# Kernel tuning notes

Measured on AMD Instinct MI355X. Metric: run time of the kernel, lower is better.

The kernel has to match this reference:

```python
import jax, jax.numpy as jnp
import numpy as np

B, H, S, D = 2, 12, 2048, 64

def setup_inputs() -> dict:
    key = jax.random.key(0)
    kq, kk, kv = jax.random.split(key, 3)
    Q = jax.random.normal(kq, (B, H, S, D), dtype=jnp.float32)
    K = jax.random.normal(kk, (B, H, S, D), dtype=jnp.float32)
    V = jax.random.normal(kv, (B, H, S, D), dtype=jnp.float32)
    return {"Q": Q, "K": K, "V": V}

def reference(Q, K, V):
    # NOTE: original code scales by sqrt(Q.shape[-2]) (the sequence length),
    # not the head dim — reproduced faithfully.
    scale = 1.0 / np.sqrt(Q.shape[-2]).astype(np.float32)
    scores = jnp.einsum('bhqd,bhkd->bhqk', Q, K) * scale  # [B,H,S,S]
    attn = jax.nn.softmax(scores, axis=-1)
    context = jnp.einsum('bhqk,bhkd->bhqd', attn, V)      # [B,H,S,D]
    # torch .squeeze(-1) only removes the last dim if it is size 1; D=64 so no-op
    return context
```

## Files before the change

kernel.cpp:

```cpp
#include <hip/hip_runtime.h>
#include <hip/hip_bf16.h>
#include <math.h>
#include <stdint.h>

#define BATCH 2
#define NH 12
#define SEQ 2048
#define HD 64
#define TQ 64
#define TK 64
#define NHEADS (BATCH*NH)
#define NIT (SEQ / TK)

typedef short bf16x8 __attribute__((ext_vector_type(8)));
typedef float f32x4 __attribute__((ext_vector_type(4)));
typedef float f32x16 __attribute__((ext_vector_type(16)));
typedef unsigned short us4_t __attribute__((ext_vector_type(4)));
typedef unsigned short us8_t __attribute__((ext_vector_type(8)));
typedef unsigned int u32x4 __attribute__((ext_vector_type(4)));

#if __has_builtin(__builtin_amdgcn_exp2f)
#define EXP2F(x) __builtin_amdgcn_exp2f(x)
#else
#define EXP2F(x) exp2f(x)
#endif

static __device__ __forceinline__ unsigned short f2bf(float f) {
    unsigned int u = __float_as_uint(f);
    u += 0x7fffu + ((u >> 16) & 1u);
    return (unsigned short)(u >> 16);
}

static __device__ __forceinline__ unsigned int pack2bf(float a, float b) {
    __hip_bfloat162 v = __float22bfloat162_rn(float2{a, b});
    return *(unsigned int*)&v;
}

static __device__ __forceinline__ void async_cp16(const void* g, void* l) {
    __builtin_amdgcn_global_load_lds(
        (const __attribute__((address_space(1))) void*)g,
        (__attribute__((address_space(3))) void*)(uintptr_t)l,
        16, 0, 0);
}

static __device__ __forceinline__ int tile_off(int r, int c) {
    int rp  = r >> 1;
    int pos = (((r & 1) << 3) | c) ^ (rp & 15);
    return rp * 128 + pos * 8;
}

__global__ __launch_bounds__(256)
void prep_kv(const float* __restrict__ K, const float* __restrict__ V,
             unsigned short* __restrict__ Kb, unsigned short* __restrict__ Vtb) {
    __shared__ unsigned short T[64][66];
    const int bh = blockIdx.x >> 5;
    const int s0 = (blockIdx.x & 31) * 64;
    const int tid = threadIdx.x;
    const size_t off = ((size_t)bh * SEQ + s0) * HD;

    #pragma unroll
    for (int u = 0; u < 4; ++u) {
        int idx = u * 1024 + tid * 4;
        float4 a = *(const float4*)&K[off + idx];
        us4_t r4 = { f2bf(a.x), f2bf(a.y), f2bf(a.z), f2bf(a.w) };
        *(us4_t*)&Kb[off + idx] = r4;
    }
    #pragma unroll
    for (int u = 0; u < 4; ++u) {
        int idx = u * 1024 + tid * 4;
        int r = idx >> 6, col = idx & 63;
        float4 a = *(const float4*)&V[off + idx];
        *(unsigned int*)&T[r][col]     = pack2bf(a.x, a.y);
        *(unsigned int*)&T[r][col + 2] = pack2bf(a.z, a.w);
    }
    __syncthreads();
    unsigned short* Vdst = Vtb + (size_t)bh * HD * SEQ;
    const int g = tid & 7, dd = tid >> 3;
    #pragma unroll
    for (int h = 0; h < 2; ++h) {
        int d = dd + 32 * h;
        us8_t r8;
        #pragma unroll
        for (int j = 0; j < 8; ++j) {
            int src = ((g >> 1) << 4) + ((j >> 2) << 3) + ((g & 1) << 2) + (j & 3);
            r8[j] = T[src][d];
        }
        *(us8_t*)&Vdst[(size_t)d * SEQ + s0 + g * 8] = r8;
    }
}

__global__ __launch_bounds__(256, 3)
void fa_main(const float* __restrict__ Q,
             const unsigned short* __restrict__ Kb,
             const unsigned short* __restrict__ Vtb,
             float* __restrict__ O, float qs) {
    const int x  = blockIdx.x & 7;
    const int t  = blockIdx.x >> 3;
    const int bh = x + 8 * (t % 3);
    const int qt = t / 3;
    const int q0 = qt * TQ;

    __shared__ __align__(16) unsigned char SH[49664];
    float* Lsum = (float*)(SH + 49152);
    float* Linv = (float*)(SH + 49408);
    float* ORed = (float*)SH;
    unsigned short* QS = (unsigned short*)(SH + 32768);

    const int tid  = threadIdx.x;
    const int w    = tid >> 6;
    const int mt   = w >> 1;
    const int nt   = w & 1;
    const int lane = tid & 63;
    const int l31  = lane & 31;
    const int hi   = lane >> 5;

    const float*          Qh = Q   + ((size_t)bh * SEQ + q0) * HD;
    const unsigned short* Kh = Kb  + (size_t)bh * SEQ * HD;
    const unsigned short* Vh = Vtb + (size_t)bh * HD * SEQ;

    int rS[2], cS[2];
    #pragma unroll
    for (int i = 0; i < 2; ++i) {
        int rp = w * 8 + 4 * i + (lane >> 4);
        int lc = (lane & 15) ^ (rp & 15);
        rS[i] = 2 * rp + (lc >> 3);
        cS[i] = lc & 7;
    }
    const int dst0 = (w * 8 + 0) * 128, dst1 = (w * 8 + 4) * 128;
    const size_t kG0 = (size_t)rS[0] * HD  + cS[0] * 8;
    const size_t kG1 = (size_t)rS[1] * HD  + cS[1] * 8;
    const size_t vG0 = (size_t)rS[0] * SEQ + cS[0] * 8;
    const size_t vG1 = (size_t)rS[1] * SEQ + cS[1] * 8;

    {
        unsigned short* K0 = (unsigned short*)(SH);
        unsigned short* V0 = (unsigned short*)(SH + 8192);
        async_cp16(Kh + kG0, &K0[dst0]);
        async_cp16(Kh + kG1, &K0[dst1]);
        async_cp16(Vh + vG0, &V0[dst0]);
        async_cp16(Vh + vG1, &V0[dst1]);
    }
    #pragma unroll
    for (int u = 0; u < 4; ++u) {
        int idx = u * 1024 + tid * 4;
        int r = idx >> 6, col = idx & 63;
        float4 a = *(const float4*)&Qh[idx];
        uint2 pk = { pack2bf(a.x * qs, a.y * qs), pack2bf(a.z * qs, a.w * qs) };
        *(uint2*)&QS[tile_off(r, col >> 3) + (col & 7)] = pk;
    }
    __syncthreads();

    bf16x8 qf[4];
    #pragma unroll
    for (int s = 0; s < 4; ++s)
        qf[s] = *(const bf16x8*)&QS[tile_off(mt * 32 + l31, s * 2 + hi)];
    __syncthreads();

    {
        unsigned short* K1 = (unsigned short*)(SH + 16384);
        unsigned short* V1 = (unsigned short*)(SH + 16384 + 8192);
        async_cp16(Kh + (size_t)TK * HD + kG0, &K1[dst0]);
        async_cp16(Kh + (size_t)TK * HD + kG1, &K1[dst1]);
        async_cp16(Vh + (size_t)TK + vG0,      &V1[dst0]);
        async_cp16(Vh + (size_t)TK + vG1,      &V1[dst1]);
    }

    int kOffL[4], vOffL[2][2];
    #pragma unroll
    for (int s = 0; s < 4; ++s) kOffL[s] = tile_off(nt * 32 + l31, s * 2 + hi);
    #pragma unroll
    for (int dt = 0; dt < 2; ++dt)
        #pragma unroll
        for (int ks = 0; ks < 2; ++ks)
            vOffL[dt][ks] = tile_off(dt * 32 + l31, nt * 4 + ks * 2 + hi);

    f32x16 o[2];
    o[0] = (f32x16)(0.f);
    o[1] = (f32x16)(0.f);
    float lsum = 0.f;

    auto FIN = [&](const f32x16& sp, const bf16x8 (&vp)[2][2]) {
        float e0[8], e1[8];
        #pragma unroll
        for (int r = 0; r < 8; ++r) e0[r] = EXP2F(sp[r]);
        #pragma unroll
        for (int r = 0; r < 8; ++r) e1[r] = EXP2F(sp[8 + r]);
        union { u32x4 d; bf16x8 h; } pu0, pu1;
        pu0.d = (u32x4){ pack2bf(e0[0], e0[1]), pack2bf(e0[2], e0[3]),
                         pack2bf(e0[4], e0[5]), pack2bf(e0[6], e0[7]) };
        pu1.d = (u32x4){ pack2bf(e1[0], e1[1]), pack2bf(e1[2], e1[3]),
                         pack2bf(e1[4], e1[5]), pack2bf(e1[6], e1[7]) };
        bf16x8 pf0 = pu0.h, pf1 = pu1.h;
        o[0] = __builtin_amdgcn_mfma_f32_32x32x16_bf16(pf0, vp[0][0], o[0], 0, 0, 0);
        o[1] = __builtin_amdgcn_mfma_f32_32x32x16_bf16(pf0, vp[1][0], o[1], 0, 0, 0);
        o[0] = __builtin_amdgcn_mfma_f32_32x32x16_bf16(pf1, vp[0][1], o[0], 0, 0, 0);
        o[1] = __builtin_amdgcn_mfma_f32_32x32x16_bf16(pf1, vp[1][1], o[1], 0, 0, 0);
        float t0 = ((e0[0] + e0[1]) + (e0[2] + e0[3]))
                 + ((e0[4] + e0[5]) + (e0[6] + e0[7]));
        float t1 = ((e1[0] + e1[1]) + (e1[2] + e1[3]))
                 + ((e1[4] + e1[5]) + (e1[6] + e1[7]));
        lsum += t0 + t1;
    };

    unsigned int b0 = 0, b1 = 16384, b2 = 32768;

    f32x16 scp;
    bf16x8 vfp[2][2];

    {
        unsigned short* Kn = (unsigned short*)(SH + b2);
        unsigned short* Vn = (unsigned short*)(SH + b2 + 8192);
        async_cp16(Kh + (size_t)2 * TK * HD + kG0, &Kn[dst0]);
        async_cp16(Kh + (size_t)2 * TK * HD + kG1, &Kn[dst1]);
        async_cp16(Vh + (size_t)2 * TK + vG0,      &Vn[dst0]);
        async_cp16(Vh + (size_t)2 * TK + vG1,      &Vn[dst1]);

        const unsigned short* Ks = (const unsigned short*)(SH + b0);
        const unsigned short* Vs = (const unsigned short*)(SH + b0 + 8192);
        #pragma unroll
        for (int dt = 0; dt < 2; ++dt)
            #pragma unroll
            for (int ks = 0; ks < 2; ++ks)
                vfp[dt][ks] = *(const bf16x8*)&Vs[vOffL[dt][ks]];
        f32x16 sc = (f32x16)(0.f);
        #pragma unroll
        for (int s = 0; s < 4; ++s) {
            bf16x8 kf = *(const bf16x8*)&Ks[kOffL[s]];
            sc = __builtin_amdgcn_mfma_f32_32x32x16_bf16(kf, qf[s], sc, 0, 0, 0);
        }
        scp = sc;
        unsigned int btmp = b0; b0 = b1; b1 = b2; b2 = btmp;
    }

    #pragma unroll 2
    for (int it = 1; it < NIT; ++it) {
        asm volatile("s_waitcnt lgkmcnt(0)" ::: "memory");
        if (it == NIT - 1) { asm volatile("s_waitcnt vmcnt(0)" ::: "memory"); }
        else               { asm volatile("s_waitcnt vmcnt(4)" ::: "memory"); }
        __builtin_amdgcn_s_barrier();

        const unsigned short* Ks = (const unsigned short*)(SH + b0);
        const unsigned short* Vs = (const unsigned short*)(SH + b0 + 8192);

        bf16x8 kfc[4];
        #pragma unroll
        for (int s = 0; s < 4; ++s)
            kfc[s] = *(const bf16x8*)&Ks[kOffL[s]];
        bf16x8 vfc[2][2];
        #pragma unroll
        for (int dt = 0; dt < 2; ++dt)
            #pragma unroll
            for (int ks = 0; ks < 2; ++ks)
                vfc[dt][ks] = *(const bf16x8*)&Vs[vOffL[dt][ks]];

        if (it + 2 < NIT) {
            const size_t kv = (size_t)(it + 2) * TK;
            unsigned short* Kn = (unsigned short*)(SH + b2);
            unsigned short* Vn = (unsigned short*)(SH + b2 + 8192);
            async_cp16(Kh + kv * HD + kG0, &Kn[dst0]);
            async_cp16(Kh + kv * HD + kG1, &Kn[dst1]);
            async_cp16(Vh + kv + vG0,      &Vn[dst0]);
            async_cp16(Vh + kv + vG1,      &Vn[dst1]);
        }

        FIN(scp, vfp);

        f32x16 scc = (f32x16)(0.f);
        #pragma unroll
        for (int s = 0; s < 4; ++s)
            scc = __builtin_amdgcn_mfma_f32_32x32x16_bf16(kfc[s], qf[s], scc, 0, 0, 0);

        scp = scc;
        #pragma unroll
        for (int dt = 0; dt < 2; ++dt)
            #pragma unroll
            for (int ks = 0; ks < 2; ++ks)
                vfp[dt][ks] = vfc[dt][ks];

        unsigned int btmp = b0; b0 = b1; b1 = b2; b2 = btmp;
    }

    FIN(scp, vfp);

    lsum += __shfl_xor(lsum, 32, 64);

    if (nt == 1) {
        if (lane < 32) Lsum[mt * 32 + lane] = lsum;
        #pragma unroll
        for (int dt = 0; dt < 2; ++dt) {
            const int d = dt * 32 + l31;
            #pragma unroll
            for (int g = 0; g < 4; ++g) {
                const int m0 = mt * 32 + 8 * g + 4 * hi;
                const int ph = (m0 >> 2) ^ (d & 15);
                float4 v = { o[dt][4*g+0], o[dt][4*g+1], o[dt][4*g+2], o[dt][4*g+3] };
                *(float4*)&ORed[d * 64 + ph * 4] = v;
            }
        }
    }
    __syncthreads();

    if (nt == 0) {
        float ltot = lsum + Lsum[mt * 32 + l31];
        if (lane < 32) Linv[mt * 32 + lane] = 1.0f / ltot;
        float* Oh = O + ((size_t)bh * SEQ + q0) * HD;
        #pragma unroll
        for (int dt = 0; dt < 2; ++dt) {
            const int d = dt * 32 + l31;
            #pragma unroll
            for (int g = 0; g < 4; ++g) {
                const int m0 = mt * 32 + 8 * g + 4 * hi;
                const int ph = (m0 >> 2) ^ (d & 15);
                float4 part = *(const float4*)&ORed[d * 64 + ph * 4];
                float4 inv4 = *(const float4*)&Linv[m0];
                const float* pp = (const float*)&part;
                const float* ii = (const float*)&inv4;
                #pragma unroll
                for (int j = 0; j < 4; ++j)
                    Oh[(size_t)(m0 + j) * HD + d] = (o[dt][4*g+j] + pp[j]) * ii[j];
            }
        }
    }
}

#define PAD 8
#define LSTR (HD + PAD)

__global__ __launch_bounds__(256)
void fa_fwd_fb(const float* __restrict__ Q, const float* __restrict__ K,
               const float* __restrict__ V, float* __restrict__ O) {
    const int x  = blockIdx.x & 7;
    const int t  = blockIdx.x >> 3;
    const int bh = x + 8 * (t % 3);
    const int qt = t / 3;
    const int q0 = qt * TQ;
    const long base = (long)bh * SEQ * HD;

    __shared__ unsigned short Qs[TQ][LSTR];
    __shared__ unsigned short Ks2[64][LSTR];
    __shared__ unsigned short Vt[HD][64 + PAD];
    __shared__ unsigned short Ps2[4][16][LSTR];

    const int tid  = threadIdx.x;
    const int wave = tid >> 6;
    const int lane = tid & 63;
    const int col  = lane & 15;
    const int quad = lane >> 4;
    const int m0   = wave * 16;

    #pragma unroll
    for (int i = 0; i < 4; ++i) {
        int idx = tid + 256 * i;
        int row = idx >> 4;
        int c4  = (idx & 15) * 4;
        float4 v = *(const float4*)&Q[base + (long)(q0 + row) * HD + c4];
        ushort4 b = { f2bf(v.x), f2bf(v.y), f2bf(v.z), f2bf(v.w) };
        *(ushort4*)&Qs[row][c4] = b;
    }
    __syncthreads();

    bf16x8 aq0 = *(const bf16x8*)&Qs[m0 + col][quad * 8];
    bf16x8 aq1 = *(const bf16x8*)&Qs[m0 + col][32 + quad * 8];

    f32x4 o0 = {0.f,0.f,0.f,0.f}, o1 = o0, o2 = o0, o3 = o0;
    float l[4] = {0.f, 0.f, 0.f, 0.f};
    const float scale = 0.022097086912079608f;

    for (int kv0 = 0; kv0 < SEQ; kv0 += 64) {
        __syncthreads();
        #pragma unroll
        for (int i = 0; i < 4; ++i) {
            int idx = tid + 256 * i;
            int row = idx >> 4;
            int c4  = (idx & 15) * 4;
            float4 kv = *(const float4*)&K[base + (long)(kv0 + row) * HD + c4];
            ushort4 kb = { f2bf(kv.x), f2bf(kv.y), f2bf(kv.z), f2bf(kv.w) };
            *(ushort4*)&Ks2[row][c4] = kb;
            float4 vv = *(const float4*)&V[base + (long)(kv0 + row) * HD + c4];
            Vt[c4 + 0][row] = f2bf(vv.x);
            Vt[c4 + 1][row] = f2bf(vv.y);
            Vt[c4 + 2][row] = f2bf(vv.z);
            Vt[c4 + 3][row] = f2bf(vv.w);
        }
        __syncthreads();

        f32x4 sc[4];
        #pragma unroll
        for (int n = 0; n < 4; ++n) {
            bf16x8 b0 = *(const bf16x8*)&Ks2[n * 16 + col][quad * 8];
            bf16x8 b1 = *(const bf16x8*)&Ks2[n * 16 + col][32 + quad * 8];
            f32x4 acc = {0.f,0.f,0.f,0.f};
            acc = __builtin_amdgcn_mfma_f32_16x16x32_bf16(aq0, b0, acc, 0, 0, 0);
            acc = __builtin_amdgcn_mfma_f32_16x16x32_bf16(aq1, b1, acc, 0, 0, 0);
            sc[n] = acc;
        }

        float tsum[4] = {0.f, 0.f, 0.f, 0.f};
        #pragma unroll
        for (int n = 0; n < 4; ++n) {
            #pragma unroll
            for (int r = 0; r < 4; ++r) {
                float p = __expf(sc[n][r] * scale);
                tsum[r] += p;
                Ps2[wave][quad * 4 + r][n * 16 + col] = f2bf(p);
            }
        }
        #pragma unroll
        for (int off = 1; off < 16; off <<= 1) {
            #pragma unroll
            for (int r = 0; r < 4; ++r) tsum[r] += __shfl_xor(tsum[r], off, 64);
        }
        #pragma unroll
        for (int r = 0; r < 4; ++r) l[r] += tsum[r];

        bf16x8 ap0 = *(const bf16x8*)&Ps2[wave][col][quad * 8];
        bf16x8 ap1 = *(const bf16x8*)&Ps2[wave][col][32 + quad * 8];
        #pragma unroll
        for (int n = 0; n < 4; ++n) {
            bf16x8 b0 = *(const bf16x8*)&Vt[n * 16 + col][quad * 8];
            bf16x8 b1 = *(const bf16x8*)&Vt[n * 16 + col][32 + quad * 8];
            f32x4* op = (n == 0) ? &o0 : (n == 1) ? &o1 : (n == 2) ? &o2 : &o3;
            *op = __builtin_amdgcn_mfma_f32_16x16x32_bf16(ap0, b0, *op, 0, 0, 0);
            *op = __builtin_amdgcn_mfma_f32_16x16x32_bf16(ap1, b1, *op, 0, 0, 0);
        }
    }

    float inv[4];
    #pragma unroll
    for (int r = 0; r < 4; ++r) inv[r] = 1.0f / l[r];
    #pragma unroll
    for (int r = 0; r < 4; ++r) {
        long row = base + (long)(q0 + m0 + quad * 4 + r) * HD;
        O[row +  0 + col] = o0[r] * inv[r];
        O[row + 16 + col] = o1[r] * inv[r];
        O[row + 32 + col] = o2[r] * inv[r];
        O[row + 48 + col] = o3[r] * inv[r];
    }
}

extern "C" void kernel_launch(void* const* d_in, const int* in_sizes, int n_in,
                              void* d_out, int out_size, void* d_ws, size_t ws_size,
                              hipStream_t stream) {
    const float* Q = (const float*)d_in[0];
    const float* K = (const float*)d_in[1];
    const float* V = (const float*)d_in[2];
    float* O = (float*)d_out;

    const size_t tensorElems = (size_t)NHEADS * SEQ * HD;
    const size_t need = 2 * tensorElems * sizeof(unsigned short);

    if (ws_size >= need) {
        unsigned short* Kb  = (unsigned short*)d_ws;
        unsigned short* Vtb = Kb + tensorElems;
        const float qs = (float)(1.4426950408889634 / sqrt(2048.0));
        prep_kv<<<dim3(NHEADS * (SEQ / 64)), dim3(256), 0, stream>>>(K, V, Kb, Vtb);
        fa_main<<<dim3(NHEADS * (SEQ / TQ)), dim3(256), 0, stream>>>(Q, Kb, Vtb, O, qs);
    } else {
        fa_fwd_fb<<<dim3(NHEADS * (SEQ / TQ)), dim3(256), 0, stream>>>(Q, K, V, O);
    }
}
```

Baseline: 114.7 us.

## Fuse K bf16 conversion into attention loop and raise MFMA wave priority

Drops the K conversion from the prep kernel. The attention kernel now loads fp32 K straight from global memory into registers one tile ahead, packs it to bf16 and writes it into the swizzled LDS buffer itself, while V keeps the async global-to-LDS path. This removes one workspace buffer and one pass of K writes and reads. In exchange, every query tile block now reads fp32 K, which is twice the bytes of bf16 K and is repeated across 32 query tiles, and the K stage adds register pressure. It also wraps the MFMA groups in s_setprio to favour matrix issue across waves.

Result: slower. 121.9 us (+6.2%).

```diff
diff --git a/kernel.cpp b/kernel.cpp
--- a/kernel.cpp
+++ b/kernel.cpp
@@ -50,21 +50,13 @@
 }
 
 __global__ __launch_bounds__(256)
-void prep_kv(const float* __restrict__ K, const float* __restrict__ V,
-             unsigned short* __restrict__ Kb, unsigned short* __restrict__ Vtb) {
+void prep_v(const float* __restrict__ V, unsigned short* __restrict__ Vtb) {
     __shared__ unsigned short T[64][66];
     const int bh = blockIdx.x >> 5;
     const int s0 = (blockIdx.x & 31) * 64;
     const int tid = threadIdx.x;
     const size_t off = ((size_t)bh * SEQ + s0) * HD;
 
-    #pragma unroll
-    for (int u = 0; u < 4; ++u) {
-        int idx = u * 1024 + tid * 4;
-        float4 a = *(const float4*)&K[off + idx];
-        us4_t r4 = { f2bf(a.x), f2bf(a.y), f2bf(a.z), f2bf(a.w) };
-        *(us4_t*)&Kb[off + idx] = r4;
-    }
     #pragma unroll
     for (int u = 0; u < 4; ++u) {
         int idx = u * 1024 + tid * 4;
@@ -90,8 +82,7 @@
 }
 
 __global__ __launch_bounds__(256, 3)
-void fa_main(const float* __restrict__ Q,
-             const unsigned short* __restrict__ Kb,
+void fa_main(const float* __restrict__ Q, const float* __restrict__ K,
              const unsigned short* __restrict__ Vtb,
              float* __restrict__ O, float qs) {
     const int x  = blockIdx.x & 7;
@@ -114,9 +105,9 @@
     const int l31  = lane & 31;
     const int hi   = lane >> 5;
 
-    const float*          Qh = Q   + ((size_t)bh * SEQ + q0) * HD;
-    const unsigned short* Kh = Kb  + (size_t)bh * SEQ * HD;
-    const unsigned short* Vh = Vtb + (size_t)bh * HD * SEQ;
+    const float*          Qh  = Q   + ((size_t)bh * SEQ + q0) * HD;
+    const float*          KhF = K   + (size_t)bh * SEQ * HD;
+    const unsigned short* Vh  = Vtb + (size_t)bh * HD * SEQ;
 
     int rS[2], cS[2];
     #pragma unroll
@@ -131,14 +122,30 @@
     const size_t kG1 = (size_t)rS[1] * HD  + cS[1] * 8;
     const size_t vG0 = (size_t)rS[0] * SEQ + cS[0] * 8;
     const size_t vG1 = (size_t)rS[1] * SEQ + cS[1] * 8;
-
+    const int ldsK0 = dst0 + lane * 8;
+    const int ldsK1 = dst1 + lane * 8;
+
+    auto stageK = [&](const float4& a0, const float4& a1,
+                      const float4& b0f, const float4& b1f, unsigned short* Kn) {
+        u32x4 w0 = { pack2bf(a0.x, a0.y), pack2bf(a0.z, a0.w),
+                     pack2bf(a1.x, a1.y), pack2bf(a1.z, a1.w) };
+        u32x4 w1 = { pack2bf(b0f.x, b0f.y), pack2bf(b0f.z, b0f.w),
+                     pack2bf(b1f.x, b1f.y), pack2bf(b1f.z, b1f.w) };
+        *(u32x4*)&Kn[ldsK0] = w0;
+        *(u32x4*)&Kn[ldsK1] = w1;
+    };
+
+    float4 ka0 = *(const float4*)&KhF[kG0];
+    float4 ka1 = *(const float4*)&KhF[kG0 + 4];
+    float4 kb0 = *(const float4*)&KhF[kG1];
+    float4 kb1 = *(const float4*)&KhF[kG1 + 4];
     {
-        unsigned short* K0 = (unsigned short*)(SH);
         unsigned short* V0 = (unsigned short*)(SH + 8192);
-        async_cp16(Kh + kG0, &K0[dst0]);
-        async_cp16(Kh + kG1, &K0[dst1]);
         async_cp16(Vh + vG0, &V0[dst0]);
         async_cp16(Vh + vG1, &V0[dst1]);
+        unsigned short* V1 = (unsigned short*)(SH + 16384 + 8192);
+        async_cp16(Vh + (size_t)TK + vG0, &V1[dst0]);
+        async_cp16(Vh + (size_t)TK + vG1, &V1[dst1]);
     }
     #pragma unroll
     for (int u = 0; u < 4; ++u) {
@@ -148,6 +155,7 @@
         uint2 pk = { pack2bf(a.x * qs, a.y * qs), pack2bf(a.z * qs, a.w * qs) };
         *(uint2*)&QS[tile_off(r, col >> 3) + (col & 7)] = pk;
     }
+    stageK(ka0, ka1, kb0, kb1, (unsigned short*)SH);
     __syncthreads();
 
     bf16x8 qf[4];
@@ -155,15 +163,6 @@
     for (int s = 0; s < 4; ++s)
         qf[s] = *(const bf16x8*)&QS[tile_off(mt * 32 + l31, s * 2 + hi)];
     __syncthreads();
-
-    {
-        unsigned short* K1 = (unsigned short*)(SH + 16384);
-        unsigned short* V1 = (unsigned short*)(SH + 16384 + 8192);
-        async_cp16(Kh + (size_t)TK * HD + kG0, &K1[dst0]);
-        async_cp16(Kh + (size_t)TK * HD + kG1, &K1[dst1]);
-        async_cp16(Vh + (size_t)TK + vG0,      &V1[dst0]);
-        async_cp16(Vh + (size_t)TK + vG1,      &V1[dst1]);
-    }
 
     int kOffL[4], vOffL[2][2];
     #pragma unroll
@@ -191,10 +190,12 @@
         pu1.d = (u32x4){ pack2bf(e1[0], e1[1]), pack2bf(e1[2], e1[3]),
                          pack2bf(e1[4], e1[5]), pack2bf(e1[6], e1[7]) };
         bf16x8 pf0 = pu0.h, pf1 = pu1.h;
+        __builtin_amdgcn_s_setprio(1);
         o[0] = __builtin_amdgcn_mfma_f32_32x32x16_bf16(pf0, vp[0][0], o[0], 0, 0, 0);
         o[1] = __builtin_amdgcn_mfma_f32_32x32x16_bf16(pf0, vp[1][0], o[1], 0, 0, 0);
         o[0] = __builtin_amdgcn_mfma_f32_32x32x16_bf16(pf1, vp[0][1], o[0], 0, 0, 0);
         o[1] = __builtin_amdgcn_mfma_f32_32x32x16_bf16(pf1, vp[1][1], o[1], 0, 0, 0);
+        __builtin_amdgcn_s_setprio(0);
         float t0 = ((e0[0] + e0[1]) + (e0[2] + e0[3]))
                  + ((e0[4] + e0[5]) + (e0[6] + e0[7]));
         float t1 = ((e1[0] + e1[1]) + (e1[2] + e1[3]))
@@ -208,35 +209,42 @@
     bf16x8 vfp[2][2];
 
     {
-        unsigned short* Kn = (unsigned short*)(SH + b2);
-        unsigned short* Vn = (unsigned short*)(SH + b2 + 8192);
-        async_cp16(Kh + (size_t)2 * TK * HD + kG0, &Kn[dst0]);
-        async_cp16(Kh + (size_t)2 * TK * HD + kG1, &Kn[dst1]);
-        async_cp16(Vh + (size_t)2 * TK + vG0,      &Vn[dst0]);
-        async_cp16(Vh + (size_t)2 * TK + vG1,      &Vn[dst1]);
-
         const unsigned short* Ks = (const unsigned short*)(SH + b0);
         const unsigned short* Vs = (const unsigned short*)(SH + b0 + 8192);
+        bf16x8 kfc[4];
+        #pragma unroll
+        for (int s = 0; s < 4; ++s) kfc[s] = *(const bf16x8*)&Ks[kOffL[s]];
         #pragma unroll
         for (int dt = 0; dt < 2; ++dt)
             #pragma unroll
             for (int ks = 0; ks < 2; ++ks)
                 vfp[dt][ks] = *(const bf16x8*)&Vs[vOffL[dt][ks]];
+
+        ka0 = *(const float4*)&KhF[(size_t)TK * HD + kG0];
+        ka1 = *(const float4*)&KhF[(size_t)TK * HD + kG0 + 4];
+        kb0 = *(const float4*)&KhF[(size_t)TK * HD + kG1];
+        kb1 = *(const float4*)&KhF[(size_t)TK * HD + kG1 + 4];
+        {
+            unsigned short* Vn = (unsigned short*)(SH + b2 + 8192);
+            async_cp16(Vh + (size_t)2 * TK + vG0, &Vn[dst0]);
+            async_cp16(Vh + (size_t)2 * TK + vG1, &Vn[dst1]);
+        }
+
         f32x16 sc = (f32x16)(0.f);
-        #pragma unroll
-        for (int s = 0; s < 4; ++s) {
-            bf16x8 kf = *(const bf16x8*)&Ks[kOffL[s]];
-            sc = __builtin_amdgcn_mfma_f32_32x32x16_bf16(kf, qf[s], sc, 0, 0, 0);
-        }
+        __builtin_amdgcn_s_setprio(1);
+        #pragma unroll
+        for (int s = 0; s < 4; ++s)
+            sc = __builtin_amdgcn_mfma_f32_32x32x16_bf16(kfc[s], qf[s], sc, 0, 0, 0);
+        __builtin_amdgcn_s_setprio(0);
         scp = sc;
+
+        stageK(ka0, ka1, kb0, kb1, (unsigned short*)(SH + b1));
         unsigned int btmp = b0; b0 = b1; b1 = b2; b2 = btmp;
     }
 
     #pragma unroll 2
     for (int it = 1; it < NIT; ++it) {
-        asm volatile("s_waitcnt lgkmcnt(0)" ::: "memory");
-        if (it == NIT - 1) { asm volatile("s_waitcnt vmcnt(0)" ::: "memory"); }
-        else               { asm volatile("s_waitcnt vmcnt(4)" ::: "memory"); }
+        asm volatile("s_waitcnt vmcnt(2) lgkmcnt(0)" ::: "memory");
         __builtin_amdgcn_s_barrier();
 
         const unsigned short* Ks = (const unsigned short*)(SH + b0);
@@ -244,8 +252,7 @@
 
         bf16x8 kfc[4];
         #pragma unroll
-        for (int s = 0; s < 4; ++s)
-            kfc[s] = *(const bf16x8*)&Ks[kOffL[s]];
+        for (int s = 0; s < 4; ++s) kfc[s] = *(const bf16x8*)&Ks[kOffL[s]];
         bf16x8 vfc[2][2];
         #pragma unroll
         for (int dt = 0; dt < 2; ++dt)
@@ -253,22 +260,31 @@
             for (int ks = 0; ks < 2; ++ks)
                 vfc[dt][ks] = *(const bf16x8*)&Vs[vOffL[dt][ks]];
 
+        if (it + 1 < NIT) {
+            const size_t kv = (size_t)(it + 1) * TK;
+            ka0 = *(const float4*)&KhF[kv * HD + kG0];
+            ka1 = *(const float4*)&KhF[kv * HD + kG0 + 4];
+            kb0 = *(const float4*)&KhF[kv * HD + kG1];
+            kb1 = *(const float4*)&KhF[kv * HD + kG1 + 4];
+        }
         if (it + 2 < NIT) {
             const size_t kv = (size_t)(it + 2) * TK;
-            unsigned short* Kn = (unsigned short*)(SH + b2);
             unsigned short* Vn = (unsigned short*)(SH + b2 + 8192);
-            async_cp16(Kh + kv * HD + kG0, &Kn[dst0]);
-            async_cp16(Kh + kv * HD + kG1, &Kn[dst1]);
-            async_cp16(Vh + kv + vG0,      &Vn[dst0]);
-            async_cp16(Vh + kv + vG1,      &Vn[dst1]);
+            async_cp16(Vh + kv + vG0, &Vn[dst0]);
+            async_cp16(Vh + kv + vG1, &Vn[dst1]);
         }
 
         FIN(scp, vfp);
 
         f32x16 scc = (f32x16)(0.f);
+        __builtin_amdgcn_s_setprio(1);
         #pragma unroll
         for (int s = 0; s < 4; ++s)
             scc = __builtin_amdgcn_mfma_f32_32x32x16_bf16(kfc[s], qf[s], scc, 0, 0, 0);
+        __builtin_amdgcn_s_setprio(0);
+
+        if (it + 1 < NIT)
+            stageK(ka0, ka1, kb0, kb1, (unsigned short*)(SH + b1));
 
         scp = scc;
         #pragma unroll
@@ -447,14 +463,13 @@
     float* O = (float*)d_out;
 
     const size_t tensorElems = (size_t)NHEADS * SEQ * HD;
-    const size_t need = 2 * tensorElems * sizeof(unsigned short);
+    const size_t need = tensorElems * sizeof(unsigned short);
 
     if (ws_size >= need) {
-        unsigned short* Kb  = (unsigned short*)d_ws;
-        unsigned short* Vtb = Kb + tensorElems;
+        unsigned short* Vtb = (unsigned short*)d_ws;
         const float qs = (float)(1.4426950408889634 / sqrt(2048.0));
-        prep_kv<<<dim3(NHEADS * (SEQ / 64)), dim3(256), 0, stream>>>(K, V, Kb, Vtb);
-        fa_main<<<dim3(NHEADS * (SEQ / TQ)), dim3(256), 0, stream>>>(Q, Kb, Vtb, O, qs);
+        prep_v<<<dim3(NHEADS * (SEQ / 64)), dim3(256), 0, stream>>>(V, Vtb);
+        fa_main<<<dim3(NHEADS * (SEQ / TQ)), dim3(256), 0, stream>>>(Q, K, Vtb, O, qs);
     } else {
         fa_fwd_fb<<<dim3(NHEADS * (SEQ / TQ)), dim3(256), 0, stream>>>(Q, K, V, O);
     }
```
